# Kernel tuning notes

Measured on AMD Instinct MI355X. Metric: run time of the kernel, lower is better.

The kernel has to match this reference:

```python
import jax, jax.numpy as jnp
import numpy as np

# skeletal graph constants
CONN_A = np.array([0,1,2,0,4,5,0,7,8,0,10,11,0,13,14])
CONN_B = np.array([1,2,3,4,5,6,7,8,9,10,11,12,13,14,15])
# angle-limited joints with their (parent, child) from the connection lists
ANG_J = np.array([11,14,5,8]); ANG_P = np.array([10,13,4,7]); ANG_C = np.array([12,15,6,9])


def setup_inputs() -> dict:
    key = jax.random.key(0)
    ks = jax.random.split(key, 16)
    B, T, J, C = 64, 243, 17, 128
    def lin(k, fin, fout):
        kw, kb = jax.random.split(k)
        s = 1.0 / np.sqrt(fin)
        return (jax.random.uniform(kw, (fin, fout), jnp.float32, -s, s),
                jax.random.uniform(kb, (fout,), jnp.float32, -s, s))
    aw1, ab1 = lin(ks[0], C, C // 2)
    aw2, ab2 = lin(ks[1], C // 2, 3)
    bw1, bb1 = lin(ks[2], 2 * C, C)
    bw2, bb2 = lin(ks[3], C, 1)
    cw1, cb1 = lin(ks[4], C * J, 64)
    cw2, cb2 = lin(ks[5], 64, 8)
    return {
        "features": jax.random.normal(ks[6], (B, T, J, C), jnp.float32),
        "pose3d": jax.random.normal(ks[7], (B, T, J, 3), jnp.float32),
        "aw1": aw1, "ab1": ab1, "aw2": aw2, "ab2": ab2,
        "bw1": bw1, "bb1": bb1, "bw2": bw2, "bb2": bb2,
        "cw1": cw1, "cb1": cb1, "cw2": cw2, "cb2": cb2,
    }


def _gelu(x):
    return jax.nn.gelu(x, approximate=False)


def reference(features, pose3d, aw1, ab1, aw2, ab2, bw1, bb1, bw2, bb2, cw1, cb1, cw2, cb2):
    B, T, J, C = features.shape
    # angle predictor: Linear -> GELU -> Linear on every joint feature
    predicted_angles = _gelu(features @ aw1 + ab1) @ aw2 + ab2  # [B,T,J,3]

    # actual bone lengths: vectorized gather over 15 connections
    vec = pose3d[:, :, CONN_B, :] - pose3d[:, :, CONN_A, :]       # [B,T,15,3]
    actual_bone_lengths = jnp.linalg.norm(vec, axis=-1, keepdims=True)  # [B,T,15,1]

    # bone features: concat endpoint features, small MLP
    bone_feat = jnp.concatenate([features[:, :, CONN_A, :], features[:, :, CONN_B, :]], axis=-1)  # [B,T,15,2C]
    predicted_bone_lengths = jax.nn.relu(_gelu(bone_feat @ bw1 + bb1) @ bw2 + bb2)  # [B,T,15,1]

    # actual joint angles at the 4 angle-limited joints, zeros elsewhere
    v1 = pose3d[:, :, ANG_J, :] - pose3d[:, :, ANG_P, :]
    v2 = pose3d[:, :, ANG_C, :] - pose3d[:, :, ANG_J, :]
    v1 = v1 / (jnp.linalg.norm(v1, axis=-1, keepdims=True) + 1e-10)
    v2 = v2 / (jnp.linalg.norm(v2, axis=-1, keepdims=True) + 1e-10)
    dot = jnp.clip(jnp.sum(v1 * v2, axis=-1, keepdims=True), -1 + 1e-7, 1 - 1e-7)
    angle = jnp.arccos(dot)  # [B,T,4,1]
    actual_angles = jnp.zeros((B, T, J, 1), features.dtype).at[:, :, ANG_J, :].set(angle)

    # action classifier on time-averaged flattened joint features
    action_feat = features.reshape(B, T, J * C).mean(axis=1)  # [B,J*C]
    action_logits = _gelu(action_feat @ cw1 + cb1) @ cw2 + cb2  # [B,8]

    return (predicted_angles, actual_angles, predicted_bone_lengths, actual_bone_lengths, action_logits)
```

## Files before the change

kernel.cpp:

```cpp
#include <hip/hip_runtime.h>
#include <math.h>

#define NF 15552
#define NJ 17
#define NC 128
#define JC (NJ*NC)
#define TT 243
#define FB 8

constexpr int cA[15] = {0,1,2,0,4,5,0,7,8,0,10,11,0,13,14};
constexpr int cB[15] = {1,2,3,4,5,6,7,8,9,10,11,12,13,14,15};
constexpr int aJ[4] = {11,14,5,8};
constexpr int aP[4] = {10,13,4,7};
constexpr int aCc[4] = {12,15,6,9};

__device__ const int d_cA16[16] = {0,1,2,0,4,5,0,7,8,0,10,11,0,13,14,0};
__device__ const int d_cB16[16] = {1,2,3,4,5,6,7,8,9,10,11,12,13,14,15,0};

typedef __bf16 bf16x8 __attribute__((ext_vector_type(8)));
typedef float f32x4 __attribute__((ext_vector_type(4)));
typedef unsigned short u16x8 __attribute__((ext_vector_type(8)));

__device__ __forceinline__ float gelu_exact(float x){
  return 0.5f * x * (1.0f + erff(x * 0.7071067811865476f));
}
__device__ __forceinline__ float gelu_fast(float x){
  const float s2 = x * x;
  const float q  = fmaf(s2, -0.1029437f, -2.3021183f);
  const float e  = __builtin_amdgcn_exp2f(q * x);
  return x * __builtin_amdgcn_rcpf(1.0f + e);
}
__device__ __forceinline__ unsigned short bfc(float x){
  return __builtin_bit_cast(unsigned short, (__bf16)x);
}
__device__ __forceinline__ float bf2f(unsigned short u){
  return __builtin_bit_cast(float, ((unsigned)u) << 16);
}

__global__ __launch_bounds__(256) void k_geom(const float* __restrict__ pose,
                                              float* __restrict__ out_aa,
                                              float* __restrict__ out_abl)
{
  const int f = blockIdx.x * 256 + threadIdx.x;
  if (f >= NF) return;
  const float* p = pose + (long)f * NJ * 3;
  float px[NJ], py[NJ], pz[NJ];
  #pragma unroll
  for (int j = 0; j < NJ; ++j){ px[j] = p[3*j]; py[j] = p[3*j+1]; pz[j] = p[3*j+2]; }

  #pragma unroll
  for (int i = 0; i < 15; ++i){
    const int a = cA[i], b = cB[i];
    const float dx = px[b]-px[a], dy = py[b]-py[a], dz = pz[b]-pz[a];
    out_abl[(long)f*15 + i] = sqrtf(dx*dx + dy*dy + dz*dz);
  }

  float ang[NJ];
  #pragma unroll
  for (int j = 0; j < NJ; ++j) ang[j] = 0.0f;
  #pragma unroll
  for (int i = 0; i < 4; ++i){
    const int jj = aJ[i], pp = aP[i], cc = aCc[i];
    float v1x = px[jj]-px[pp], v1y = py[jj]-py[pp], v1z = pz[jj]-pz[pp];
    float v2x = px[cc]-px[jj], v2y = py[cc]-py[jj], v2z = pz[cc]-pz[jj];
    const float n1 = sqrtf(v1x*v1x + v1y*v1y + v1z*v1z) + 1e-10f;
    const float n2 = sqrtf(v2x*v2x + v2y*v2y + v2z*v2z) + 1e-10f;
    v1x /= n1; v1y /= n1; v1z /= n1;
    v2x /= n2; v2y /= n2; v2z /= n2;
    float d = v1x*v2x + v1y*v2y + v1z*v2z;
    d = fminf(fmaxf(d, -1.0f + 1e-7f), 1.0f - 1e-7f);
    ang[jj] = acosf(d);
  }
  #pragma unroll
  for (int j = 0; j < NJ; ++j) out_aa[(long)f*NJ + j] = ang[j];
}

#define SFO(fi, off16) (((fi)*272 + (off16))*8)

__global__ __launch_bounds__(256) void k_fused(const float* __restrict__ feat,
    const float* __restrict__ aw1, const float* __restrict__ ab1,
    const float* __restrict__ aw2, const float* __restrict__ ab2,
    const float* __restrict__ bw1, const float* __restrict__ bb1,
    const float* __restrict__ bw2, const float* __restrict__ bb2,
    float* __restrict__ out_pa, float* __restrict__ out_pbl,
    float* __restrict__ mean_acc)
{
  __shared__ __align__(16) unsigned short s_feat[FB*NJ*NC];
  __shared__ float s_red[4][FB][16];

  const int tid  = threadIdx.x;
  const int w    = tid >> 6;
  const int lane = tid & 63;
  const int g    = lane >> 4;
  const int c    = lane & 15;
  const long f0  = (long)blockIdx.x * FB;

  {
    const float* base = feat + f0 * JC;
    for (int u = tid; u < FB*272; u += 256){
      const float4 v0 = *(const float4*)(base + u*8);
      const float4 v1 = *(const float4*)(base + u*8 + 4);
      u16x8 p;
      p[0]=bfc(v0.x); p[1]=bfc(v0.y); p[2]=bfc(v0.z); p[3]=bfc(v0.w);
      p[4]=bfc(v1.x); p[5]=bfc(v1.y); p[6]=bfc(v1.z); p[7]=bfc(v1.w);
      const int fi = u / 272, r = u - fi*272;
      const int j = r >> 4, kb = r & 15;
      *(u16x8*)&s_feat[SFO(fi, j*16 + (kb ^ (j & 7)))] = p;
    }
  }

  bf16x8 wb[8][2];
  float bb1c[2], bw2c[2];
  #pragma unroll
  for (int nf = 0; nf < 2; ++nf){
    const int col = w*32 + nf*16 + c;
    bb1c[nf] = bb1[col];
    bw2c[nf] = bw2[col];
    #pragma unroll
    for (int ks = 0; ks < 8; ++ks){
      u16x8 t;
      #pragma unroll
      for (int e = 0; e < 8; ++e) t[e] = bfc(bw1[(ks*32 + g*8 + e)*128 + col]);
      wb[ks][nf] = __builtin_bit_cast(bf16x8, t);
    }
  }

  const int jA = d_cA16[c], jB = d_cB16[c];
  int boff[8];
  #pragma unroll
  for (int ks = 0; ks < 8; ++ks){
    const int kk = ks*32 + g*8;
    const int j  = (kk < 128) ? jA : jB;
    const int kb = (kk < 128) ? (ks*4 + g) : (ks*4 + g - 16);
    boff[ks] = j*16 + (kb ^ (j & 7));
  }

  __syncthreads();

  f32x4 bacc[FB][2];
  #pragma unroll
  for (int fi = 0; fi < FB; ++fi){ bacc[fi][0] = (f32x4)0.0f; bacc[fi][1] = (f32x4)0.0f; }

  #pragma unroll
  for (int ks = 0; ks < 8; ++ks){
    bf16x8 av[FB];
    #pragma unroll
    for (int fi = 0; fi < FB; ++fi)
      av[fi] = __builtin_bit_cast(bf16x8, *(const u16x8*)&s_feat[SFO(fi, boff[ks])]);
    #pragma unroll
    for (int fi = 0; fi < FB; ++fi){
      bacc[fi][0] = __builtin_amdgcn_mfma_f32_16x16x32_bf16(av[fi], wb[ks][0], bacc[fi][0], 0, 0, 0);
      bacc[fi][1] = __builtin_amdgcn_mfma_f32_16x16x32_bf16(av[fi], wb[ks][1], bacc[fi][1], 0, 0, 0);
    }
  }

  #pragma unroll
  for (int fi = 0; fi < FB; ++fi){
    float s[4] = {0.f, 0.f, 0.f, 0.f};
    #pragma unroll
    for (int nf = 0; nf < 2; ++nf)
      #pragma unroll
      for (int r = 0; r < 4; ++r)
        s[r] += gelu_fast(bacc[fi][nf][r] + bb1c[nf]) * bw2c[nf];
    #pragma unroll
    for (int r = 0; r < 4; ++r){
      s[r] += __shfl_xor(s[r], 1);
      s[r] += __shfl_xor(s[r], 2);
      s[r] += __shfl_xor(s[r], 4);
      s[r] += __shfl_xor(s[r], 8);
    }
    if (c == 0)
      #pragma unroll
      for (int r = 0; r < 4; ++r) s_red[w][fi][g*4 + r] = s[r];
  }

  bf16x8 wa[4][4];
  float ab1c[4], aw2c[4][3];
  #pragma unroll
  for (int nf = 0; nf < 4; ++nf){
    const int col = nf*16 + c;
    ab1c[nf] = ab1[col];
    #pragma unroll
    for (int m = 0; m < 3; ++m) aw2c[nf][m] = aw2[col*3 + m];
    #pragma unroll
    for (int kt = 0; kt < 4; ++kt){
      u16x8 t;
      #pragma unroll
      for (int e = 0; e < 8; ++e) t[e] = bfc(aw1[(kt*32 + g*8 + e)*64 + col]);
      wa[kt][nf] = __builtin_bit_cast(bf16x8, t);
    }
  }
  const float ab2c[3] = {ab2[0], ab2[1], ab2[2]};

  const int fa0 = 2*w, fa1 = 2*w + 1;
  f32x4 acc0[4], acc1[4], accj[4];
  #pragma unroll
  for (int nf = 0; nf < 4; ++nf){ acc0[nf]=(f32x4)0.0f; acc1[nf]=(f32x4)0.0f; accj[nf]=(f32x4)0.0f; }

  #pragma unroll
  for (int kt = 0; kt < 4; ++kt){
    const int kbx = kt*4 + g;
    const bf16x8 av0 = __builtin_bit_cast(bf16x8,
        *(const u16x8*)&s_feat[SFO(fa0, c*16 + (kbx ^ (c & 7)))]);
    const bf16x8 av1 = __builtin_bit_cast(bf16x8,
        *(const u16x8*)&s_feat[SFO(fa1, c*16 + (kbx ^ (c & 7)))]);
    #pragma unroll
    for (int nf = 0; nf < 4; ++nf){
      acc0[nf] = __builtin_amdgcn_mfma_f32_16x16x32_bf16(av0, wa[kt][nf], acc0[nf], 0, 0, 0);
      acc1[nf] = __builtin_amdgcn_mfma_f32_16x16x32_bf16(av1, wa[kt][nf], acc1[nf], 0, 0, 0);
    }
    if (w == 0){
      const bf16x8 avj = __builtin_bit_cast(bf16x8,
          *(const u16x8*)&s_feat[SFO(c & 7, 16*16 + kbx)]);
      #pragma unroll
      for (int nf = 0; nf < 4; ++nf)
        accj[nf] = __builtin_amdgcn_mfma_f32_16x16x32_bf16(avj, wa[kt][nf], accj[nf], 0, 0, 0);
    }
  }

  #pragma unroll
  for (int half = 0; half < 2; ++half){
    const int fa = half ? fa1 : fa0;
    f32x4* acc = half ? acc1 : acc0;
    float s[4][3];
    #pragma unroll
    for (int r = 0; r < 4; ++r){ s[r][0]=0.f; s[r][1]=0.f; s[r][2]=0.f; }
    #pragma unroll
    for (int nf = 0; nf < 4; ++nf)
      #pragma unroll
      for (int r = 0; r < 4; ++r){
        const float h = gelu_fast(acc[nf][r] + ab1c[nf]);
        s[r][0] = fmaf(h, aw2c[nf][0], s[r][0]);
        s[r][1] = fmaf(h, aw2c[nf][1], s[r][1]);
        s[r][2] = fmaf(h, aw2c[nf][2], s[r][2]);
      }
    #pragma unroll
    for (int r = 0; r < 4; ++r)
      #pragma unroll
      for (int m = 0; m < 3; ++m){
        float v = s[r][m];
        v += __shfl_xor(v, 1);
        v += __shfl_xor(v, 2);
        v += __shfl_xor(v, 4);
        v += __shfl_xor(v, 8);
        s[r][m] = v;
      }
    if (c == 0){
      #pragma unroll
      for (int r = 0; r < 4; ++r){
        const long joint = g*4 + r;
        #pragma unroll
        for (int m = 0; m < 3; ++m)
          out_pa[((f0 + fa)*NJ + joint)*3 + m] = s[r][m] + ab2c[m];
      }
    }
  }
  if (w == 0){
    float s[4][3];
    #pragma unroll
    for (int r = 0; r < 4; ++r){ s[r][0]=0.f; s[r][1]=0.f; s[r][2]=0.f; }
    #pragma unroll
    for (int nf = 0; nf < 4; ++nf)
      #pragma unroll
      for (int r = 0; r < 4; ++r){
        const float h = gelu_fast(accj[nf][r] + ab1c[nf]);
        s[r][0] = fmaf(h, aw2c[nf][0], s[r][0]);
        s[r][1] = fmaf(h, aw2c[nf][1], s[r][1]);
        s[r][2] = fmaf(h, aw2c[nf][2], s[r][2]);
      }
    #pragma unroll
    for (int r = 0; r < 4; ++r)
      #pragma unroll
      for (int m = 0; m < 3; ++m){
        float v = s[r][m];
        v += __shfl_xor(v, 1);
        v += __shfl_xor(v, 2);
        v += __shfl_xor(v, 4);
        v += __shfl_xor(v, 8);
        s[r][m] = v;
      }
    if (c == 0 && g < 2){
      #pragma unroll
      for (int r = 0; r < 4; ++r){
        const long frame = g*4 + r;
        #pragma unroll
        for (int m = 0; m < 3; ++m)
          out_pa[((f0 + frame)*NJ + 16)*3 + m] = s[r][m] + ab2c[m];
      }
    }
  }

  __syncthreads();

  if (tid < FB*15){
    const int fi = tid / 15, row = tid - fi*15;
    const float v = s_red[0][fi][row] + s_red[1][fi][row] +
                    s_red[2][fi][row] + s_red[3][fi][row] + bb2[0];
    out_pbl[(f0 + fi)*15 + row] = fmaxf(v, 0.0f);
  }

  {
    const int b0 = (int)(f0 / TT);
    const int b1 = (int)((f0 + FB - 1) / TT);
    const int split = (b1 > b0) ? (b1*TT - (int)f0) : FB;
    for (int jc = tid; jc < JC; jc += 256){
      const int j = jc >> 7, k = jc & 127;
      const int eoff = (j*16 + ((k >> 3) ^ (j & 7)))*8 + (k & 7);
      float s0 = 0.f, s1 = 0.f;
      #pragma unroll
      for (int fi = 0; fi < FB; ++fi){
        const float v = bf2f(s_feat[fi*JC + eoff]);
        if (fi < split) s0 += v; else s1 += v;
      }
      atomicAdd(&mean_acc[(long)b0*JC + jc], s0);
      if (b1 > b0) atomicAdd(&mean_acc[(long)b1*JC + jc], s1);
    }
  }
}

__global__ __launch_bounds__(256) void k_action(const float* __restrict__ sum_src,
    const float* __restrict__ cw1, const float* __restrict__ cb1,
    const float* __restrict__ cw2, const float* __restrict__ cb2,
    float* __restrict__ out_lg)
{
  __shared__ float s_m[JC];
  __shared__ float s_part[4][64];
  __shared__ float s_h[64];
  const int b = blockIdx.x, tid = threadIdx.x;
  for (int i = tid; i < JC; i += 256) s_m[i] = sum_src[(long)b*JC + i] * (1.0f/243.0f);
  __syncthreads();
  const int n = tid & 63, part = tid >> 6;
  float s = 0.0f;
  const int k0 = part * 544;
  for (int k = k0; k < k0 + 544; ++k) s = fmaf(s_m[k], cw1[(long)k*64 + n], s);
  s_part[part][n] = s;
  __syncthreads();
  if (tid < 64) s_h[tid] = gelu_exact(s_part[0][tid] + s_part[1][tid] +
                                      s_part[2][tid] + s_part[3][tid] + cb1[tid]);
  __syncthreads();
  if (tid < 8){
    float v = cb2[tid];
    #pragma unroll
    for (int k = 0; k < 64; ++k) v = fmaf(s_h[k], cw2[k*8 + tid], v);
    out_lg[b*8 + tid] = v;
  }
}

extern "C" void kernel_launch(void* const* d_in, const int* in_sizes, int n_in,
                              void* d_out, int out_size, void* d_ws, size_t ws_size,
                              hipStream_t stream)
{
  const float* feat = (const float*)d_in[0];
  const float* pose = (const float*)d_in[1];
  const float* aw1  = (const float*)d_in[2];
  const float* ab1  = (const float*)d_in[3];
  const float* aw2  = (const float*)d_in[4];
  const float* ab2  = (const float*)d_in[5];
  const float* bw1  = (const float*)d_in[6];
  const float* bb1  = (const float*)d_in[7];
  const float* bw2  = (const float*)d_in[8];
  const float* bb2  = (const float*)d_in[9];
  const float* cw1  = (const float*)d_in[10];
  const float* cb1  = (const float*)d_in[11];
  const float* cw2  = (const float*)d_in[12];
  const float* cb2  = (const float*)d_in[13];

  float* out = (float*)d_out;
  float* out_pa  = out;
  float* out_aa  = out + 793152;
  float* out_pbl = out + 1057536;
  float* out_abl = out + 1290816;
  float* out_lg  = out + 1524096;

  float* mean_acc = (float*)d_ws;
  hipMemsetAsync(mean_acc, 0, (size_t)64 * JC * sizeof(float), stream);

  k_geom<<<dim3((NF + 255)/256), dim3(256), 0, stream>>>(pose, out_aa, out_abl);
  k_fused<<<dim3(NF/FB), dim3(256), 0, stream>>>(feat, aw1, ab1, aw2, ab2,
                                                 bw1, bb1, bw2, bb2,
                                                 out_pa, out_pbl, mean_acc);
  k_action<<<dim3(64), dim3(256), 0, stream>>>(mean_acc, cw1, cb1, cw2, cb2, out_lg);
}
```

Measured before the change: 146.9 us.

## Restructure fused kernel into warp-specialized streaming without shared memory

Moves the bf16 weight conversion into a separate prep kernel that writes MFMA-ready fragments to workspace. The fused kernel now uses 5 waves: one wave handles the angle MLP and the per-batch feature sums, and four waves handle the bone MLP. All of them read features directly from global memory instead of staging them in LDS. Bone-length partial sums are accumulated with atomics into zeroed output, and a separate fixup kernel adds the bias and ReLU. Zeroing moves from memset into the geometry kernel. The change removes LDS staging and the per-block weight conversion, but features are now read multiple times from global memory, and it adds atomics and extra launches.

```diff
diff --git a/kernel.cpp b/kernel.cpp
--- a/kernel.cpp
+++ b/kernel.cpp
@@ -4,9 +4,10 @@
 #define NF 15552
 #define NJ 17
 #define NC 128
-#define JC (NJ*NC)
+#define JC 2176
 #define TT 243
-#define FB 8
+#define FPB 12
+#define GRID_FUSED (NF/FPB)
 
 constexpr int cA[15] = {0,1,2,0,4,5,0,7,8,0,10,11,0,13,14};
 constexpr int cB[15] = {1,2,3,4,5,6,7,8,9,10,11,12,13,14,15};
@@ -21,6 +22,9 @@
 typedef float f32x4 __attribute__((ext_vector_type(4)));
 typedef unsigned short u16x8 __attribute__((ext_vector_type(8)));
 
+#define WSO_WB 557056
+#define WSO_WA 622592
+
 __device__ __forceinline__ float gelu_exact(float x){
   return 0.5f * x * (1.0f + erff(x * 0.7071067811865476f));
 }
@@ -33,289 +37,301 @@
 __device__ __forceinline__ unsigned short bfc(float x){
   return __builtin_bit_cast(unsigned short, (__bf16)x);
 }
-__device__ __forceinline__ float bf2f(unsigned short u){
-  return __builtin_bit_cast(float, ((unsigned)u) << 16);
+
+__global__ __launch_bounds__(256) void k_prep(const float* __restrict__ bw1,
+                                              const float* __restrict__ aw1,
+                                              unsigned short* __restrict__ ws_wb,
+                                              unsigned short* __restrict__ ws_wa)
+{
+  const int u = blockIdx.x*256 + threadIdx.x;
+  if (u < 4096){
+    const int lane = u & 63, ks = (u>>6)&7, nf = (u>>9)&1, widx = u>>10;
+    const int c = lane & 15, g = lane >> 4;
+    const int col = widx*32 + nf*16 + c;
+    u16x8 t;
+    #pragma unroll
+    for (int e = 0; e < 8; ++e) t[e] = bfc(bw1[(ks*32 + g*8 + e)*128 + col]);
+    *(u16x8*)&ws_wb[u*8] = t;
+  } else if (u < 4096 + 1024){
+    const int v = u - 4096;
+    const int lane = v & 63, nf = (v>>6)&3, kt = v>>8;
+    const int c = lane & 15, g = lane >> 4;
+    const int col = nf*16 + c;
+    u16x8 t;
+    #pragma unroll
+    for (int e = 0; e < 8; ++e) t[e] = bfc(aw1[(kt*32 + g*8 + e)*64 + col]);
+    *(u16x8*)&ws_wa[v*8] = t;
+  }
 }
 
 __global__ __launch_bounds__(256) void k_geom(const float* __restrict__ pose,
                                               float* __restrict__ out_aa,
-                                              float* __restrict__ out_abl)
-{
-  const int f = blockIdx.x * 256 + threadIdx.x;
-  if (f >= NF) return;
-  const float* p = pose + (long)f * NJ * 3;
-  float px[NJ], py[NJ], pz[NJ];
-  #pragma unroll
-  for (int j = 0; j < NJ; ++j){ px[j] = p[3*j]; py[j] = p[3*j+1]; pz[j] = p[3*j+2]; }
-
-  #pragma unroll
-  for (int i = 0; i < 15; ++i){
-    const int a = cA[i], b = cB[i];
-    const float dx = px[b]-px[a], dy = py[b]-py[a], dz = pz[b]-pz[a];
-    out_abl[(long)f*15 + i] = sqrtf(dx*dx + dy*dy + dz*dz);
+                                              float* __restrict__ out_abl,
+                                              float* __restrict__ out_pbl,
+                                              float* __restrict__ mean_acc)
+{
+  __shared__ float sp[256*51];
+  const int tid = threadIdx.x;
+  const int fbase = blockIdx.x * 256;
+  const int nfr = min(256, NF - fbase);
+
+  for (int u = tid; u < nfr*51; u += 256) sp[u] = pose[(long)fbase*51 + u];
+  for (long i = (long)blockIdx.x*256 + tid; i < (long)NF*15; i += (long)gridDim.x*256)
+    out_pbl[i] = 0.0f;
+  for (long i = (long)blockIdx.x*256 + tid; i < 64L*JC; i += (long)gridDim.x*256)
+    mean_acc[i] = 0.0f;
+  __syncthreads();
+
+  if (tid < nfr){
+    const int f = fbase + tid;
+    const float* p = sp + tid*51;
+    float px[NJ], py[NJ], pz[NJ];
+    #pragma unroll
+    for (int j = 0; j < NJ; ++j){ px[j] = p[3*j]; py[j] = p[3*j+1]; pz[j] = p[3*j+2]; }
+
+    #pragma unroll
+    for (int i = 0; i < 15; ++i){
+      const int a = cA[i], b = cB[i];
+      const float dx = px[b]-px[a], dy = py[b]-py[a], dz = pz[b]-pz[a];
+      out_abl[(long)f*15 + i] = sqrtf(dx*dx + dy*dy + dz*dz);
+    }
+
+    float ang[NJ];
+    #pragma unroll
+    for (int j = 0; j < NJ; ++j) ang[j] = 0.0f;
+    #pragma unroll
+    for (int i = 0; i < 4; ++i){
+      const int jj = aJ[i], pp = aP[i], cc = aCc[i];
+      float v1x = px[jj]-px[pp], v1y = py[jj]-py[pp], v1z = pz[jj]-pz[pp];
+      float v2x = px[cc]-px[jj], v2y = py[cc]-py[jj], v2z = pz[cc]-pz[jj];
+      const float n1 = sqrtf(v1x*v1x + v1y*v1y + v1z*v1z) + 1e-10f;
+      const float n2 = sqrtf(v2x*v2x + v2y*v2y + v2z*v2z) + 1e-10f;
+      v1x /= n1; v1y /= n1; v1z /= n1;
+      v2x /= n2; v2y /= n2; v2z /= n2;
+      float d = v1x*v2x + v1y*v2y + v1z*v2z;
+      d = fminf(fmaxf(d, -1.0f + 1e-7f), 1.0f - 1e-7f);
+      ang[jj] = acosf(d);
+    }
+    #pragma unroll
+    for (int j = 0; j < NJ; ++j) out_aa[(long)f*NJ + j] = ang[j];
   }
-
-  float ang[NJ];
-  #pragma unroll
-  for (int j = 0; j < NJ; ++j) ang[j] = 0.0f;
-  #pragma unroll
-  for (int i = 0; i < 4; ++i){
-    const int jj = aJ[i], pp = aP[i], cc = aCc[i];
-    float v1x = px[jj]-px[pp], v1y = py[jj]-py[pp], v1z = pz[jj]-pz[pp];
-    float v2x = px[cc]-px[jj], v2y = py[cc]-py[jj], v2z = pz[cc]-pz[jj];
-    const float n1 = sqrtf(v1x*v1x + v1y*v1y + v1z*v1z) + 1e-10f;
-    const float n2 = sqrtf(v2x*v2x + v2y*v2y + v2z*v2z) + 1e-10f;
-    v1x /= n1; v1y /= n1; v1z /= n1;
-    v2x /= n2; v2y /= n2; v2z /= n2;
-    float d = v1x*v2x + v1y*v2y + v1z*v2z;
-    d = fminf(fmaxf(d, -1.0f + 1e-7f), 1.0f - 1e-7f);
-    ang[jj] = acosf(d);
-  }
-  #pragma unroll
-  for (int j = 0; j < NJ; ++j) out_aa[(long)f*NJ + j] = ang[j];
-}
-
-#define SFO(fi, off16) (((fi)*272 + (off16))*8)
-
-__global__ __launch_bounds__(256) void k_fused(const float* __restrict__ feat,
-    const float* __restrict__ aw1, const float* __restrict__ ab1,
-    const float* __restrict__ aw2, const float* __restrict__ ab2,
-    const float* __restrict__ bw1, const float* __restrict__ bb1,
-    const float* __restrict__ bw2, const float* __restrict__ bb2,
+}
+
+__global__ __launch_bounds__(320) void k_fused(const float* __restrict__ feat,
+    const float* __restrict__ ab1, const float* __restrict__ aw2,
+    const float* __restrict__ ab2,
+    const float* __restrict__ bb1, const float* __restrict__ bw2,
+    const unsigned short* __restrict__ ws_wb,
+    const unsigned short* __restrict__ ws_wa,
     float* __restrict__ out_pa, float* __restrict__ out_pbl,
     float* __restrict__ mean_acc)
 {
-  __shared__ __align__(16) unsigned short s_feat[FB*NJ*NC];
-  __shared__ float s_red[4][FB][16];
-
   const int tid  = threadIdx.x;
   const int w    = tid >> 6;
   const int lane = tid & 63;
   const int g    = lane >> 4;
   const int c    = lane & 15;
-  const long f0  = (long)blockIdx.x * FB;
-
-  {
-    const float* base = feat + f0 * JC;
-    for (int u = tid; u < FB*272; u += 256){
-      const float4 v0 = *(const float4*)(base + u*8);
-      const float4 v1 = *(const float4*)(base + u*8 + 4);
-      u16x8 p;
-      p[0]=bfc(v0.x); p[1]=bfc(v0.y); p[2]=bfc(v0.z); p[3]=bfc(v0.w);
-      p[4]=bfc(v1.x); p[5]=bfc(v1.y); p[6]=bfc(v1.z); p[7]=bfc(v1.w);
-      const int fi = u / 272, r = u - fi*272;
-      const int j = r >> 4, kb = r & 15;
-      *(u16x8*)&s_feat[SFO(fi, j*16 + (kb ^ (j & 7)))] = p;
-    }
-  }
-
-  bf16x8 wb[8][2];
-  float bb1c[2], bw2c[2];
-  #pragma unroll
-  for (int nf = 0; nf < 2; ++nf){
-    const int col = w*32 + nf*16 + c;
-    bb1c[nf] = bb1[col];
-    bw2c[nf] = bw2[col];
-    #pragma unroll
-    for (int ks = 0; ks < 8; ++ks){
-      u16x8 t;
-      #pragma unroll
-      for (int e = 0; e < 8; ++e) t[e] = bfc(bw1[(ks*32 + g*8 + e)*128 + col]);
-      wb[ks][nf] = __builtin_bit_cast(bf16x8, t);
-    }
-  }
-
-  const int jA = d_cA16[c], jB = d_cB16[c];
-  int boff[8];
-  #pragma unroll
-  for (int ks = 0; ks < 8; ++ks){
-    const int kk = ks*32 + g*8;
-    const int j  = (kk < 128) ? jA : jB;
-    const int kb = (kk < 128) ? (ks*4 + g) : (ks*4 + g - 16);
-    boff[ks] = j*16 + (kb ^ (j & 7));
-  }
-
-  __syncthreads();
-
-  f32x4 bacc[FB][2];
-  #pragma unroll
-  for (int fi = 0; fi < FB; ++fi){ bacc[fi][0] = (f32x4)0.0f; bacc[fi][1] = (f32x4)0.0f; }
-
-  #pragma unroll
-  for (int ks = 0; ks < 8; ++ks){
-    bf16x8 av[FB];
-    #pragma unroll
-    for (int fi = 0; fi < FB; ++fi)
-      av[fi] = __builtin_bit_cast(bf16x8, *(const u16x8*)&s_feat[SFO(fi, boff[ks])]);
-    #pragma unroll
-    for (int fi = 0; fi < FB; ++fi){
-      bacc[fi][0] = __builtin_amdgcn_mfma_f32_16x16x32_bf16(av[fi], wb[ks][0], bacc[fi][0], 0, 0, 0);
-      bacc[fi][1] = __builtin_amdgcn_mfma_f32_16x16x32_bf16(av[fi], wb[ks][1], bacc[fi][1], 0, 0, 0);
-    }
-  }
-
-  #pragma unroll
-  for (int fi = 0; fi < FB; ++fi){
-    float s[4] = {0.f, 0.f, 0.f, 0.f};
-    #pragma unroll
-    for (int nf = 0; nf < 2; ++nf)
+  const long F0  = (long)blockIdx.x * FPB;
+
+  if (w == 0){
+    float ab1c[4], aw2c[4][3];
+    #pragma unroll
+    for (int nf = 0; nf < 4; ++nf){
+      const int col = nf*16 + c;
+      ab1c[nf] = ab1[col];
+      #pragma unroll
+      for (int m = 0; m < 3; ++m) aw2c[nf][m] = aw2[col*3 + m];
+    }
+    const float ab2c[3] = {ab2[0], ab2[1], ab2[2]};
+
+    float macc[4][8];
+    float macc16[8];
+    #pragma unroll
+    for (int kt = 0; kt < 4; ++kt)
+      #pragma unroll
+      for (int e = 0; e < 8; ++e) macc[kt][e] = 0.0f;
+    #pragma unroll
+    for (int e = 0; e < 8; ++e) macc16[e] = 0.0f;
+
+    const int b0 = (int)(F0 / TT);
+    const long bsplit = (long)(b0 + 1) * TT;
+    int curb = b0;
+
+    auto flushMean = [&](int batch){
+      float* ma = mean_acc + (long)batch*JC;
+      #pragma unroll
+      for (int kt = 0; kt < 4; ++kt)
+        #pragma unroll
+        for (int e = 0; e < 8; ++e){
+          atomicAdd(&ma[c*128 + kt*32 + g*8 + e], macc[kt][e]);
+          macc[kt][e] = 0.0f;
+        }
+      if (c < 4){
+        #pragma unroll
+        for (int e = 0; e < 8; ++e) atomicAdd(&ma[2048 + c*32 + g*8 + e], macc16[e]);
+      }
+      #pragma unroll
+      for (int e = 0; e < 8; ++e) macc16[e] = 0.0f;
+    };
+
+    for (int f = 0; f < FPB; ++f){
+      const long frame = F0 + f;
+      if (frame == bsplit){ flushMean(b0); curb = b0 + 1; }
+      const float* fb = feat + frame*JC;
+
+      f32x4 accJ[4], accX[4];
+      #pragma unroll
+      for (int nf = 0; nf < 4; ++nf){ accJ[nf] = (f32x4)0.0f; accX[nf] = (f32x4)0.0f; }
+
+      #pragma unroll
+      for (int kt = 0; kt < 4; ++kt){
+        const float* pj = fb + c*128 + kt*32 + g*8;
+        const float4 a0 = *(const float4*)pj;
+        const float4 a1 = *(const float4*)(pj + 4);
+        macc[kt][0]+=a0.x; macc[kt][1]+=a0.y; macc[kt][2]+=a0.z; macc[kt][3]+=a0.w;
+        macc[kt][4]+=a1.x; macc[kt][5]+=a1.y; macc[kt][6]+=a1.z; macc[kt][7]+=a1.w;
+        u16x8 ta;
+        ta[0]=bfc(a0.x); ta[1]=bfc(a0.y); ta[2]=bfc(a0.z); ta[3]=bfc(a0.w);
+        ta[4]=bfc(a1.x); ta[5]=bfc(a1.y); ta[6]=bfc(a1.z); ta[7]=bfc(a1.w);
+        const bf16x8 av = __builtin_bit_cast(bf16x8, ta);
+        const float* px = fb + 16*128 + kt*32 + g*8;
+        const float4 x0 = *(const float4*)px;
+        const float4 x1 = *(const float4*)(px + 4);
+        if (kt == (c & 3)){
+          macc16[0]+=x0.x; macc16[1]+=x0.y; macc16[2]+=x0.z; macc16[3]+=x0.w;
+          macc16[4]+=x1.x; macc16[5]+=x1.y; macc16[6]+=x1.z; macc16[7]+=x1.w;
+        }
+        u16x8 tx;
+        tx[0]=bfc(x0.x); tx[1]=bfc(x0.y); tx[2]=bfc(x0.z); tx[3]=bfc(x0.w);
+        tx[4]=bfc(x1.x); tx[5]=bfc(x1.y); tx[6]=bfc(x1.z); tx[7]=bfc(x1.w);
+        const bf16x8 avx = __builtin_bit_cast(bf16x8, tx);
+
+        #pragma unroll
+        for (int nf = 0; nf < 4; ++nf){
+          const bf16x8 wf = __builtin_bit_cast(bf16x8,
+              *(const u16x8*)&ws_wa[((kt*4 + nf)*64 + lane)*8]);
+          accJ[nf] = __builtin_amdgcn_mfma_f32_16x16x32_bf16(av,  wf, accJ[nf], 0, 0, 0);
+          accX[nf] = __builtin_amdgcn_mfma_f32_16x16x32_bf16(avx, wf, accX[nf], 0, 0, 0);
+        }
+      }
+
+      float s[4][3];
+      #pragma unroll
+      for (int r = 0; r < 4; ++r){ s[r][0]=0.f; s[r][1]=0.f; s[r][2]=0.f; }
+      float s16[3] = {0.f, 0.f, 0.f};
+      #pragma unroll
+      for (int nf = 0; nf < 4; ++nf){
+        #pragma unroll
+        for (int r = 0; r < 4; ++r){
+          const float h = gelu_fast(accJ[nf][r] + ab1c[nf]);
+          s[r][0] = fmaf(h, aw2c[nf][0], s[r][0]);
+          s[r][1] = fmaf(h, aw2c[nf][1], s[r][1]);
+          s[r][2] = fmaf(h, aw2c[nf][2], s[r][2]);
+        }
+        const float hx = gelu_fast(accX[nf][0] + ab1c[nf]);
+        s16[0] = fmaf(hx, aw2c[nf][0], s16[0]);
+        s16[1] = fmaf(hx, aw2c[nf][1], s16[1]);
+        s16[2] = fmaf(hx, aw2c[nf][2], s16[2]);
+      }
       #pragma unroll
       for (int r = 0; r < 4; ++r)
-        s[r] += gelu_fast(bacc[fi][nf][r] + bb1c[nf]) * bw2c[nf];
-    #pragma unroll
-    for (int r = 0; r < 4; ++r){
-      s[r] += __shfl_xor(s[r], 1);
-      s[r] += __shfl_xor(s[r], 2);
-      s[r] += __shfl_xor(s[r], 4);
-      s[r] += __shfl_xor(s[r], 8);
-    }
-    if (c == 0)
-      #pragma unroll
-      for (int r = 0; r < 4; ++r) s_red[w][fi][g*4 + r] = s[r];
-  }
-
-  bf16x8 wa[4][4];
-  float ab1c[4], aw2c[4][3];
-  #pragma unroll
-  for (int nf = 0; nf < 4; ++nf){
-    const int col = nf*16 + c;
-    ab1c[nf] = ab1[col];
-    #pragma unroll
-    for (int m = 0; m < 3; ++m) aw2c[nf][m] = aw2[col*3 + m];
-    #pragma unroll
-    for (int kt = 0; kt < 4; ++kt){
-      u16x8 t;
-      #pragma unroll
-      for (int e = 0; e < 8; ++e) t[e] = bfc(aw1[(kt*32 + g*8 + e)*64 + col]);
-      wa[kt][nf] = __builtin_bit_cast(bf16x8, t);
-    }
-  }
-  const float ab2c[3] = {ab2[0], ab2[1], ab2[2]};
-
-  const int fa0 = 2*w, fa1 = 2*w + 1;
-  f32x4 acc0[4], acc1[4], accj[4];
-  #pragma unroll
-  for (int nf = 0; nf < 4; ++nf){ acc0[nf]=(f32x4)0.0f; acc1[nf]=(f32x4)0.0f; accj[nf]=(f32x4)0.0f; }
-
-  #pragma unroll
-  for (int kt = 0; kt < 4; ++kt){
-    const int kbx = kt*4 + g;
-    const bf16x8 av0 = __builtin_bit_cast(bf16x8,
-        *(const u16x8*)&s_feat[SFO(fa0, c*16 + (kbx ^ (c & 7)))]);
-    const bf16x8 av1 = __builtin_bit_cast(bf16x8,
-        *(const u16x8*)&s_feat[SFO(fa1, c*16 + (kbx ^ (c & 7)))]);
-    #pragma unroll
-    for (int nf = 0; nf < 4; ++nf){
-      acc0[nf] = __builtin_amdgcn_mfma_f32_16x16x32_bf16(av0, wa[kt][nf], acc0[nf], 0, 0, 0);
-      acc1[nf] = __builtin_amdgcn_mfma_f32_16x16x32_bf16(av1, wa[kt][nf], acc1[nf], 0, 0, 0);
-    }
-    if (w == 0){
-      const bf16x8 avj = __builtin_bit_cast(bf16x8,
-          *(const u16x8*)&s_feat[SFO(c & 7, 16*16 + kbx)]);
-      #pragma unroll
-      for (int nf = 0; nf < 4; ++nf)
-        accj[nf] = __builtin_amdgcn_mfma_f32_16x16x32_bf16(avj, wa[kt][nf], accj[nf], 0, 0, 0);
-    }
-  }
-
-  #pragma unroll
-  for (int half = 0; half < 2; ++half){
-    const int fa = half ? fa1 : fa0;
-    f32x4* acc = half ? acc1 : acc0;
-    float s[4][3];
-    #pragma unroll
-    for (int r = 0; r < 4; ++r){ s[r][0]=0.f; s[r][1]=0.f; s[r][2]=0.f; }
-    #pragma unroll
-    for (int nf = 0; nf < 4; ++nf)
-      #pragma unroll
-      for (int r = 0; r < 4; ++r){
-        const float h = gelu_fast(acc[nf][r] + ab1c[nf]);
-        s[r][0] = fmaf(h, aw2c[nf][0], s[r][0]);
-        s[r][1] = fmaf(h, aw2c[nf][1], s[r][1]);
-        s[r][2] = fmaf(h, aw2c[nf][2], s[r][2]);
-      }
-    #pragma unroll
-    for (int r = 0; r < 4; ++r)
+        #pragma unroll
+        for (int m = 0; m < 3; ++m){
+          float v = s[r][m];
+          v += __shfl_xor(v, 1);
+          v += __shfl_xor(v, 2);
+          v += __shfl_xor(v, 4);
+          v += __shfl_xor(v, 8);
+          s[r][m] = v;
+        }
       #pragma unroll
       for (int m = 0; m < 3; ++m){
-        float v = s[r][m];
+        float v = s16[m];
         v += __shfl_xor(v, 1);
         v += __shfl_xor(v, 2);
         v += __shfl_xor(v, 4);
         v += __shfl_xor(v, 8);
-        s[r][m] = v;
-      }
-    if (c == 0){
+        s16[m] = v;
+      }
+      if (c == 0){
+        #pragma unroll
+        for (int r = 0; r < 4; ++r){
+          const int joint = g*4 + r;
+          #pragma unroll
+          for (int m = 0; m < 3; ++m)
+            out_pa[(frame*NJ + joint)*3 + m] = s[r][m] + ab2c[m];
+        }
+      }
+      if (lane == 0){
+        #pragma unroll
+        for (int m = 0; m < 3; ++m)
+          out_pa[(frame*NJ + 16)*3 + m] = s16[m] + ab2c[m];
+      }
+    }
+    flushMean(curb);
+  } else {
+    const int widx = w - 1;
+    bf16x8 wb[8][2];
+    #pragma unroll
+    for (int nf = 0; nf < 2; ++nf)
+      #pragma unroll
+      for (int ks = 0; ks < 8; ++ks)
+        wb[ks][nf] = __builtin_bit_cast(bf16x8,
+            *(const u16x8*)&ws_wb[((((widx*2 + nf)*8) + ks)*64 + lane)*8]);
+    float bb1c[2], bw2c2[2];
+    #pragma unroll
+    for (int nf = 0; nf < 2; ++nf){
+      const int col = widx*32 + nf*16 + c;
+      bb1c[nf] = bb1[col];
+      bw2c2[nf] = bw2[col];
+    }
+    const int jAo = d_cA16[c]*128, jBo = d_cB16[c]*128;
+
+    for (int f = 0; f < FPB; ++f){
+      const long frame = F0 + f;
+      const float* fb = feat + frame*JC;
+      f32x4 acc0 = (f32x4)0.0f, acc1 = (f32x4)0.0f;
+      #pragma unroll
+      for (int ks = 0; ks < 8; ++ks){
+        const int ch = (ks & 3)*32 + g*8;
+        const float* pa = fb + (ks < 4 ? jAo : jBo) + ch;
+        const float4 a0 = *(const float4*)pa;
+        const float4 a1 = *(const float4*)(pa + 4);
+        u16x8 ta;
+        ta[0]=bfc(a0.x); ta[1]=bfc(a0.y); ta[2]=bfc(a0.z); ta[3]=bfc(a0.w);
+        ta[4]=bfc(a1.x); ta[5]=bfc(a1.y); ta[6]=bfc(a1.z); ta[7]=bfc(a1.w);
+        const bf16x8 av = __builtin_bit_cast(bf16x8, ta);
+        acc0 = __builtin_amdgcn_mfma_f32_16x16x32_bf16(av, wb[ks][0], acc0, 0, 0, 0);
+        acc1 = __builtin_amdgcn_mfma_f32_16x16x32_bf16(av, wb[ks][1], acc1, 0, 0, 0);
+      }
+      float s[4];
+      #pragma unroll
+      for (int r = 0; r < 4; ++r)
+        s[r] = gelu_fast(acc0[r] + bb1c[0]) * bw2c2[0]
+             + gelu_fast(acc1[r] + bb1c[1]) * bw2c2[1];
       #pragma unroll
       for (int r = 0; r < 4; ++r){
-        const long joint = g*4 + r;
-        #pragma unroll
-        for (int m = 0; m < 3; ++m)
-          out_pa[((f0 + fa)*NJ + joint)*3 + m] = s[r][m] + ab2c[m];
+        s[r] += __shfl_xor(s[r], 1);
+        s[r] += __shfl_xor(s[r], 2);
+        s[r] += __shfl_xor(s[r], 4);
+        s[r] += __shfl_xor(s[r], 8);
+      }
+      if (c == 0){
+        #pragma unroll
+        for (int r = 0; r < 4; ++r){
+          const int bone = g*4 + r;
+          if (bone < 15) atomicAdd(&out_pbl[frame*15 + bone], s[r]);
+        }
       }
     }
   }
-  if (w == 0){
-    float s[4][3];
-    #pragma unroll
-    for (int r = 0; r < 4; ++r){ s[r][0]=0.f; s[r][1]=0.f; s[r][2]=0.f; }
-    #pragma unroll
-    for (int nf = 0; nf < 4; ++nf)
-      #pragma unroll
-      for (int r = 0; r < 4; ++r){
-        const float h = gelu_fast(accj[nf][r] + ab1c[nf]);
-        s[r][0] = fmaf(h, aw2c[nf][0], s[r][0]);
-        s[r][1] = fmaf(h, aw2c[nf][1], s[r][1]);
-        s[r][2] = fmaf(h, aw2c[nf][2], s[r][2]);
-      }
-    #pragma unroll
-    for (int r = 0; r < 4; ++r)
-      #pragma unroll
-      for (int m = 0; m < 3; ++m){
-        float v = s[r][m];
-        v += __shfl_xor(v, 1);
-        v += __shfl_xor(v, 2);
-        v += __shfl_xor(v, 4);
-        v += __shfl_xor(v, 8);
-        s[r][m] = v;
-      }
-    if (c == 0 && g < 2){
-      #pragma unroll
-      for (int r = 0; r < 4; ++r){
-        const long frame = g*4 + r;
-        #pragma unroll
-        for (int m = 0; m < 3; ++m)
-          out_pa[((f0 + frame)*NJ + 16)*3 + m] = s[r][m] + ab2c[m];
-      }
-    }
-  }
-
-  __syncthreads();
-
-  if (tid < FB*15){
-    const int fi = tid / 15, row = tid - fi*15;
-    const float v = s_red[0][fi][row] + s_red[1][fi][row] +
-                    s_red[2][fi][row] + s_red[3][fi][row] + bb2[0];
-    out_pbl[(f0 + fi)*15 + row] = fmaxf(v, 0.0f);
-  }
-
-  {
-    const int b0 = (int)(f0 / TT);
-    const int b1 = (int)((f0 + FB - 1) / TT);
-    const int split = (b1 > b0) ? (b1*TT - (int)f0) : FB;
-    for (int jc = tid; jc < JC; jc += 256){
-      const int j = jc >> 7, k = jc & 127;
-      const int eoff = (j*16 + ((k >> 3) ^ (j & 7)))*8 + (k & 7);
-      float s0 = 0.f, s1 = 0.f;
-      #pragma unroll
-      for (int fi = 0; fi < FB; ++fi){
-        const float v = bf2f(s_feat[fi*JC + eoff]);
-        if (fi < split) s0 += v; else s1 += v;
-      }
-      atomicAdd(&mean_acc[(long)b0*JC + jc], s0);
-      if (b1 > b0) atomicAdd(&mean_acc[(long)b1*JC + jc], s1);
-    }
-  }
+}
+
+__global__ __launch_bounds__(256) void k_pblfix(float* __restrict__ pbl,
+                                                const float* __restrict__ bb2)
+{
+  const long i = (long)blockIdx.x*256 + threadIdx.x;
+  if (i < (long)NF*15) pbl[i] = fmaxf(pbl[i] + bb2[0], 0.0f);
 }
 
 __global__ __launch_bounds__(256) void k_action(const float* __restrict__ sum_src,
@@ -373,11 +389,15 @@
   float* out_lg  = out + 1524096;
 
   float* mean_acc = (float*)d_ws;
-  hipMemsetAsync(mean_acc, 0, (size_t)64 * JC * sizeof(float), stream);
-
-  k_geom<<<dim3((NF + 255)/256), dim3(256), 0, stream>>>(pose, out_aa, out_abl);
-  k_fused<<<dim3(NF/FB), dim3(256), 0, stream>>>(feat, aw1, ab1, aw2, ab2,
-                                                 bw1, bb1, bw2, bb2,
-                                                 out_pa, out_pbl, mean_acc);
+  unsigned short* ws_wb = (unsigned short*)((char*)d_ws + WSO_WB);
+  unsigned short* ws_wa = (unsigned short*)((char*)d_ws + WSO_WA);
+
+  k_prep<<<dim3(20), dim3(256), 0, stream>>>(bw1, aw1, ws_wb, ws_wa);
+  k_geom<<<dim3((NF + 255)/256), dim3(256), 0, stream>>>(pose, out_aa, out_abl,
+                                                         out_pbl, mean_acc);
+  k_fused<<<dim3(GRID_FUSED), dim3(320), 0, stream>>>(feat, ab1, aw2, ab2, bb1, bw2,
+                                                      ws_wb, ws_wa,
+                                                      out_pa, out_pbl, mean_acc);
+  k_pblfix<<<dim3((NF*15 + 255)/256), dim3(256), 0, stream>>>(out_pbl, bb2);
   k_action<<<dim3(64), dim3(256), 0, stream>>>(mean_acc, cw1, cb1, cw2, cb2, out_lg);
 }
```

After: 341.3 us. 2.32x slower.
